# Performance work log

Hardware: AMD Instinct MI355X
Metric: run time of the kernel (lower is better)

Reference implementation:

```python
import jax, jax.numpy as jnp
import numpy as np

NEG_INF = -1.0e9  # matches module's negativeInfinity buffer


def setup_inputs() -> dict:
    key = jax.random.key(0)
    k0, k1, k2, k3 = jax.random.split(key, 4)
    bs, h, dh, qsl, sl = 2048, 8, 32, 64, 64
    q = jax.random.normal(k0, (bs, h, dh, qsl, 1), dtype=jnp.float32)
    k = jax.random.normal(k1, (bs, h, dh, 1, sl), dtype=jnp.float32)
    v = jax.random.normal(k2, (bs, h, dh, sl), dtype=jnp.float32)
    mask = jnp.zeros((bs, 1, qsl, sl), dtype=bool)
    gamma = jnp.ones((h,), dtype=jnp.float32)   # qk_GBN gamma
    bias = jax.random.normal(k3, (h,), dtype=jnp.float32) * 0.01  # qk_GBN bias
    return {"q": q, "k": k, "v": v, "mask": mask, "gamma": gamma, "bias": bias}


def reference(q, k, v, mask, gamma, bias):
    # scores: elementwise q*k summed over head-dim -> [bs, h, qsl, sl]
    qk = (q * k).sum(axis=2)
    # qk_GBN eval path: running m=0, s=1 -> per-head affine
    qk = qk * gamma[None, :, None, None] + bias[None, :, None, None]
    qk = jnp.where(mask, NEG_INF, qk)
    v_weights = jax.nn.softmax(qk, axis=-1)
    v_weights = jnp.where(mask, 0.0, v_weights)
    # sigmoid gating of attention weights
    v_weights = v_weights * jax.nn.sigmoid(qk)
    # output = v @ v_weights^T -> [bs, h, dvh, qsl]
    out = jnp.einsum("bhds,bhqs->bhdq", v, v_weights)
    return out
```

## Files before the change

kernel.cpp:

```cpp
#include <hip/hip_runtime.h>

typedef __attribute__((ext_vector_type(4))) float  f32x4;
typedef __attribute__((ext_vector_type(8))) __bf16 bf16x8;
typedef __attribute__((ext_vector_type(4))) __bf16 bf16x4;

#define MFMA16(a, b, c) __builtin_amdgcn_mfma_f32_16x16x32_bf16((a), (b), (c), 0, 0, 0)

__global__ __launch_bounds__(256, 8)
void mha_fused(const float* __restrict__ qg, const float* __restrict__ kg,
               const float* __restrict__ vg, const unsigned char* __restrict__ maskg,
               const float* __restrict__ gammag, const float* __restrict__ biasg,
               float* __restrict__ outg)
{
    const int bid = blockIdx.x;
    const int chunk = gridDim.x >> 3;
    const int bh = (bid & 7) * chunk + (bid >> 3);
    const int b  = bh >> 3;
    const int h  = bh & 7;
    const int t  = threadIdx.x;

    __shared__ __bf16 sKh[64][40];
    __shared__ __bf16 sKl[64][40];
    __shared__ __bf16 sV [32][72];

    const float* qb = qg + (size_t)bh * 2048;
    const float* kb = kg + (size_t)bh * 2048;
    const float* vb = vg + (size_t)bh * 2048;
    const unsigned char* mb = maskg + (size_t)b * 4096;
    float* ob = outg + (size_t)bh * 2048;

    const int w  = t >> 6;
    const int li = t & 15;
    const int hi = (t >> 4) & 3;
    const int i  = w * 16 + li;

    float qv[8];
    #pragma unroll
    for (int e = 0; e < 8; ++e) qv[e] = qb[(hi * 8 + e) * 64 + i];
    unsigned int mw[4];
    #pragma unroll
    for (int jt = 0; jt < 4; ++jt)
        mw[jt] = *(const unsigned int*)&mb[i * 64 + jt * 16 + hi * 4];

    {
        const int j = t & 63, sel = t >> 6;
        float a[8];
        #pragma unroll
        for (int e = 0; e < 8; ++e) a[e] = kb[(sel * 8 + e) * 64 + j];
        bf16x8 h8, l8;
        #pragma unroll
        for (int e = 0; e < 8; ++e) {
            __bf16 hh = (__bf16)a[e];
            h8[e] = hh;
            l8[e] = (__bf16)(a[e] - (float)hh);
        }
        const int slot = sel ^ ((j >> 3) & 3);
        *(bf16x8*)&sKh[j][slot * 8] = h8;
        *(bf16x8*)&sKl[j][slot * 8] = l8;
    }
    {
        const int d = t >> 3, j0 = (t & 7) * 8;
        f32x4 x0 = *(const f32x4*)&vb[d * 64 + j0];
        f32x4 x1 = *(const f32x4*)&vb[d * 64 + j0 + 4];
        bf16x8 vv = {(__bf16)x0[0], (__bf16)x0[1], (__bf16)x0[2], (__bf16)x0[3],
                     (__bf16)x1[0], (__bf16)x1[1], (__bf16)x1[2], (__bf16)x1[3]};
        *(bf16x8*)&sV[d][j0] = vv;
    }

    bf16x8 qh, ql;
    #pragma unroll
    for (int e = 0; e < 8; ++e) {
        __bf16 hh = (__bf16)qv[e];
        qh[e] = hh;
        ql[e] = (__bf16)(qv[e] - (float)hh);
    }

    __syncthreads();

    const float ga = gammag[h], be = biasg[h];
    float s[16];
    #pragma unroll
    for (int jt = 0; jt < 4; ++jt) {
        const int j = jt * 16 + li;
        const int slot = hi ^ ((j >> 3) & 3);
        bf16x8 ah = *(bf16x8*)&sKh[j][slot * 8];
        bf16x8 al = *(bf16x8*)&sKl[j][slot * 8];
        f32x4 c = {0.f, 0.f, 0.f, 0.f};
        c = MFMA16(al, qh, c);
        c = MFMA16(ah, ql, c);
        c = MFMA16(ah, qh, c);
        #pragma unroll
        for (int r = 0; r < 4; ++r) {
            float x = c[r] * ga + be;
            if ((mw[jt] >> (8 * r)) & 0xffu) x = -1.0e9f;
            s[jt * 4 + r] = x;
        }
    }

    float m = s[0];
    #pragma unroll
    for (int e = 1; e < 16; ++e) m = fmaxf(m, s[e]);
    m = fmaxf(m, __shfl_xor(m, 16));
    m = fmaxf(m, __shfl_xor(m, 32));
    float p[16], sum = 0.f;
    #pragma unroll
    for (int e = 0; e < 16; ++e) { p[e] = __expf(s[e] - m); sum += p[e]; }
    sum += __shfl_xor(sum, 16);
    sum += __shfl_xor(sum, 32);
    const float inv = 1.0f / sum;

    bf16x4 wv[4];
    #pragma unroll
    for (int jt = 0; jt < 4; ++jt) {
        #pragma unroll
        for (int r = 0; r < 4; ++r) {
            const int e = jt * 4 + r;
            const float g = 1.0f / (1.0f + __expf(-s[e]));
            wv[jt][r] = (__bf16)(p[e] * inv * g);
        }
    }

    f32x4 o0 = {0.f, 0.f, 0.f, 0.f};
    f32x4 o1 = {0.f, 0.f, 0.f, 0.f};
    #pragma unroll
    for (int kt = 0; kt < 2; ++kt) {
        bf16x4 wlo = wv[2 * kt], whi = wv[2 * kt + 1];
        bf16x8 wb = {wlo[0], wlo[1], wlo[2], wlo[3], whi[0], whi[1], whi[2], whi[3]};
        const int c0 = kt * 32 + hi * 4;
        const int c1 = kt * 32 + 16 + hi * 4;
        bf16x4 a0l = *(const bf16x4*)&sV[li][c0];
        bf16x4 a0h = *(const bf16x4*)&sV[li][c1];
        bf16x8 va = {a0l[0], a0l[1], a0l[2], a0l[3], a0h[0], a0h[1], a0h[2], a0h[3]};
        bf16x4 a1l = *(const bf16x4*)&sV[16 + li][c0];
        bf16x4 a1h = *(const bf16x4*)&sV[16 + li][c1];
        bf16x8 vc = {a1l[0], a1l[1], a1l[2], a1l[3], a1h[0], a1h[1], a1h[2], a1h[3]};
        o0 = MFMA16(va, wb, o0);
        o1 = MFMA16(vc, wb, o1);
    }
    #pragma unroll
    for (int r = 0; r < 4; ++r) {
        ob[(hi * 4 + r) * 64 + i]      = o0[r];
        ob[(16 + hi * 4 + r) * 64 + i] = o1[r];
    }
}

extern "C" void kernel_launch(void* const* d_in, const int* in_sizes, int n_in,
                              void* d_out, int out_size, void* d_ws, size_t ws_size,
                              hipStream_t stream)
{
    const float* q = (const float*)d_in[0];
    const float* k = (const float*)d_in[1];
    const float* v = (const float*)d_in[2];
    const unsigned char* mask = (const unsigned char*)d_in[3];
    const float* gamma = (const float*)d_in[4];
    const float* bias  = (const float*)d_in[5];
    float* out = (float*)d_out;

    const int num_bh = in_sizes[0] / 2048;
    dim3 grid(num_bh), block(256);
    hipLaunchKernelGGL(mha_fused, grid, block, 0, stream,
                       q, k, v, mask, gamma, bias, out);
}
```

Measured before the change: 110.0 us.

## Pack four heads per 1024-thread block and derive sigmoid from softmax exponentials

Each block now covers four heads of the same batch, with one 256-thread sub-block per head and per-head shared memory slices, so the grid is four times smaller. The sigmoid gate is rewritten as p/(p+exp(-m)), reusing the softmax exponential and removing one exp per element. Fewer, larger blocks cut scheduling overhead and share the mask rows across heads, but they may lower occupancy flexibility, and __syncthreads now spans 1024 threads. The algebraic sigmoid form can underflow when p and exp(-m) are both tiny.

```diff
diff --git a/kernel.cpp b/kernel.cpp
--- a/kernel.cpp
+++ b/kernel.cpp
@@ -6,22 +6,27 @@
 
 #define MFMA16(a, b, c) __builtin_amdgcn_mfma_f32_16x16x32_bf16((a), (b), (c), 0, 0, 0)
 
-__global__ __launch_bounds__(256, 8)
+__global__ __launch_bounds__(1024, 2)
 void mha_fused(const float* __restrict__ qg, const float* __restrict__ kg,
                const float* __restrict__ vg, const unsigned char* __restrict__ maskg,
                const float* __restrict__ gammag, const float* __restrict__ biasg,
                float* __restrict__ outg)
 {
-    const int bid = blockIdx.x;
+    const int bid   = blockIdx.x;
     const int chunk = gridDim.x >> 3;
-    const int bh = (bid & 7) * chunk + (bid >> 3);
-    const int b  = bh >> 3;
-    const int h  = bh & 7;
+    const int vbid  = (bid & 7) * chunk + (bid >> 3);
+    const int b  = vbid >> 1;
+    const int hg = vbid & 1;
+
     const int t  = threadIdx.x;
+    const int sb = t >> 8;
+    const int lt = t & 255;
+    const int h  = hg * 4 + sb;
+    const int bh = b * 8 + h;
 
-    __shared__ __bf16 sKh[64][40];
-    __shared__ __bf16 sKl[64][40];
-    __shared__ __bf16 sV [32][72];
+    __shared__ __bf16 sKh[4][64][40];
+    __shared__ __bf16 sKl[4][64][40];
+    __shared__ __bf16 sV [4][32][72];
 
     const float* qb = qg + (size_t)bh * 2048;
     const float* kb = kg + (size_t)bh * 2048;
@@ -29,9 +34,9 @@
     const unsigned char* mb = maskg + (size_t)b * 4096;
     float* ob = outg + (size_t)bh * 2048;
 
-    const int w  = t >> 6;
-    const int li = t & 15;
-    const int hi = (t >> 4) & 3;
+    const int w  = (lt >> 6) & 3;
+    const int li = lt & 15;
+    const int hi = (lt >> 4) & 3;
     const int i  = w * 16 + li;
 
     float qv[8];
@@ -43,7 +48,7 @@
         mw[jt] = *(const unsigned int*)&mb[i * 64 + jt * 16 + hi * 4];
 
     {
-        const int j = t & 63, sel = t >> 6;
+        const int j = lt & 63, sel = lt >> 6;
         float a[8];
         #pragma unroll
         for (int e = 0; e < 8; ++e) a[e] = kb[(sel * 8 + e) * 64 + j];
@@ -55,16 +60,16 @@
             l8[e] = (__bf16)(a[e] - (float)hh);
         }
         const int slot = sel ^ ((j >> 3) & 3);
-        *(bf16x8*)&sKh[j][slot * 8] = h8;
-        *(bf16x8*)&sKl[j][slot * 8] = l8;
+        *(bf16x8*)&sKh[sb][j][slot * 8] = h8;
+        *(bf16x8*)&sKl[sb][j][slot * 8] = l8;
     }
     {
-        const int d = t >> 3, j0 = (t & 7) * 8;
+        const int d = lt >> 3, j0 = (lt & 7) * 8;
         f32x4 x0 = *(const f32x4*)&vb[d * 64 + j0];
         f32x4 x1 = *(const f32x4*)&vb[d * 64 + j0 + 4];
         bf16x8 vv = {(__bf16)x0[0], (__bf16)x0[1], (__bf16)x0[2], (__bf16)x0[3],
                      (__bf16)x1[0], (__bf16)x1[1], (__bf16)x1[2], (__bf16)x1[3]};
-        *(bf16x8*)&sV[d][j0] = vv;
+        *(bf16x8*)&sV[sb][d][j0] = vv;
     }
 
     bf16x8 qh, ql;
@@ -83,8 +88,8 @@
     for (int jt = 0; jt < 4; ++jt) {
         const int j = jt * 16 + li;
         const int slot = hi ^ ((j >> 3) & 3);
-        bf16x8 ah = *(bf16x8*)&sKh[j][slot * 8];
-        bf16x8 al = *(bf16x8*)&sKl[j][slot * 8];
+        bf16x8 ah = *(bf16x8*)&sKh[sb][j][slot * 8];
+        bf16x8 al = *(bf16x8*)&sKl[sb][j][slot * 8];
         f32x4 c = {0.f, 0.f, 0.f, 0.f};
         c = MFMA16(al, qh, c);
         c = MFMA16(ah, ql, c);
@@ -102,9 +107,10 @@
     for (int e = 1; e < 16; ++e) m = fmaxf(m, s[e]);
     m = fmaxf(m, __shfl_xor(m, 16));
     m = fmaxf(m, __shfl_xor(m, 32));
-    float p[16], sum = 0.f;
+    const float em = __expf(-m);
+    float sum = 0.f;
     #pragma unroll
-    for (int e = 0; e < 16; ++e) { p[e] = __expf(s[e] - m); sum += p[e]; }
+    for (int e = 0; e < 16; ++e) { s[e] = __expf(s[e] - m); sum += s[e]; }
     sum += __shfl_xor(sum, 16);
     sum += __shfl_xor(sum, 32);
     const float inv = 1.0f / sum;
@@ -114,9 +120,8 @@
     for (int jt = 0; jt < 4; ++jt) {
         #pragma unroll
         for (int r = 0; r < 4; ++r) {
-            const int e = jt * 4 + r;
-            const float g = 1.0f / (1.0f + __expf(-s[e]));
-            wv[jt][r] = (__bf16)(p[e] * inv * g);
+            const float p = s[jt * 4 + r];
+            wv[jt][r] = (__bf16)(p * inv * __fdividef(p, p + em));
         }
     }
 
@@ -128,11 +133,11 @@
         bf16x8 wb = {wlo[0], wlo[1], wlo[2], wlo[3], whi[0], whi[1], whi[2], whi[3]};
         const int c0 = kt * 32 + hi * 4;
         const int c1 = kt * 32 + 16 + hi * 4;
-        bf16x4 a0l = *(const bf16x4*)&sV[li][c0];
-        bf16x4 a0h = *(const bf16x4*)&sV[li][c1];
+        bf16x4 a0l = *(const bf16x4*)&sV[sb][li][c0];
+        bf16x4 a0h = *(const bf16x4*)&sV[sb][li][c1];
         bf16x8 va = {a0l[0], a0l[1], a0l[2], a0l[3], a0h[0], a0h[1], a0h[2], a0h[3]};
-        bf16x4 a1l = *(const bf16x4*)&sV[16 + li][c0];
-        bf16x4 a1h = *(const bf16x4*)&sV[16 + li][c1];
+        bf16x4 a1l = *(const bf16x4*)&sV[sb][16 + li][c0];
+        bf16x4 a1h = *(const bf16x4*)&sV[sb][16 + li][c1];
         bf16x8 vc = {a1l[0], a1l[1], a1l[2], a1l[3], a1h[0], a1h[1], a1h[2], a1h[3]};
         o0 = MFMA16(va, wb, o0);
         o1 = MFMA16(vc, wb, o1);
@@ -157,7 +162,7 @@
     float* out = (float*)d_out;
 
     const int num_bh = in_sizes[0] / 2048;
-    dim3 grid(num_bh), block(256);
+    dim3 grid(num_bh >> 2), block(1024);
     hipLaunchKernelGGL(mha_fused, grid, block, 0, stream,
                        q, k, v, mask, gamma, bias, out);
 }
```

Measured after the change: 118.1 us. 1.07x slower.

## Stage Q/K/V/mask through LDS with vectorized loads and coalesced output stores

Applied to the files above, without the earlier changes.

Loads Q, K, V and the mask with contiguous 16-byte vector loads into shared memory, then transposes and splits them into bf16 hi/lo from LDS. Packs the mask into bit words and stages the output through LDS so the global stores are vectorized and coalesced. It also derives the sigmoid from the softmax exponentials (p/(p+e^-m)), which avoids a second exp, and drops the block-index swizzle and the occupancy hint. The cost is more LDS use, extra barriers and lower occupancy bounds.

```diff
diff --git a/kernel.cpp b/kernel.cpp
--- a/kernel.cpp
+++ b/kernel.cpp
@@ -1,80 +1,102 @@
 #include <hip/hip_runtime.h>
 
 typedef __attribute__((ext_vector_type(4))) float  f32x4;
+typedef __attribute__((ext_vector_type(2))) float  f32x2;
 typedef __attribute__((ext_vector_type(8))) __bf16 bf16x8;
 typedef __attribute__((ext_vector_type(4))) __bf16 bf16x4;
 
 #define MFMA16(a, b, c) __builtin_amdgcn_mfma_f32_16x16x32_bf16((a), (b), (c), 0, 0, 0)
 
-__global__ __launch_bounds__(256, 8)
+__global__ __launch_bounds__(256, 4)
 void mha_fused(const float* __restrict__ qg, const float* __restrict__ kg,
                const float* __restrict__ vg, const unsigned char* __restrict__ maskg,
                const float* __restrict__ gammag, const float* __restrict__ biasg,
                float* __restrict__ outg)
 {
-    const int bid = blockIdx.x;
-    const int chunk = gridDim.x >> 3;
-    const int bh = (bid & 7) * chunk + (bid >> 3);
+    const int bh = blockIdx.x;
     const int b  = bh >> 3;
     const int h  = bh & 7;
     const int t  = threadIdx.x;
 
-    __shared__ __bf16 sKh[64][40];
-    __shared__ __bf16 sKl[64][40];
-    __shared__ __bf16 sV [32][72];
+    __shared__ float              sQO[32 * 68];
+    __shared__ float              sKr[32 * 66];
+    __shared__ __bf16             sKh[64][40];
+    __shared__ __bf16             sKl[64][40];
+    __shared__ __bf16             sV [32][72];
+    __shared__ unsigned long long sMb[64];
 
     const float* qb = qg + (size_t)bh * 2048;
     const float* kb = kg + (size_t)bh * 2048;
     const float* vb = vg + (size_t)bh * 2048;
-    const unsigned char* mb = maskg + (size_t)b * 4096;
+    const unsigned char* mbp = maskg + (size_t)b * 4096;
     float* ob = outg + (size_t)bh * 2048;
 
     const int w  = t >> 6;
     const int li = t & 15;
     const int hi = (t >> 4) & 3;
     const int i  = w * 16 + li;
+    const int rd = t >> 3;
+    const int rc = (t & 7) * 8;
 
-    float qv[8];
+    {
+        f32x4 q0 = *(const f32x4*)(qb + t * 8);
+        f32x4 q1 = *(const f32x4*)(qb + t * 8 + 4);
+        f32x4 k0 = *(const f32x4*)(kb + t * 8);
+        f32x4 k1 = *(const f32x4*)(kb + t * 8 + 4);
+        f32x4 v0 = *(const f32x4*)(vb + t * 8);
+        f32x4 v1 = *(const f32x4*)(vb + t * 8 + 4);
+        uint4 mu = *(const uint4*)(mbp + t * 16);
+
+        float* qrow = &sQO[rd * 66 + rc];
+        *(f32x2*)(qrow + 0) = (f32x2){q0[0], q0[1]};
+        *(f32x2*)(qrow + 2) = (f32x2){q0[2], q0[3]};
+        *(f32x2*)(qrow + 4) = (f32x2){q1[0], q1[1]};
+        *(f32x2*)(qrow + 6) = (f32x2){q1[2], q1[3]};
+        float* krow = &sKr[rd * 66 + rc];
+        *(f32x2*)(krow + 0) = (f32x2){k0[0], k0[1]};
+        *(f32x2*)(krow + 2) = (f32x2){k0[2], k0[3]};
+        *(f32x2*)(krow + 4) = (f32x2){k1[0], k1[1]};
+        *(f32x2*)(krow + 6) = (f32x2){k1[2], k1[3]};
+
+        bf16x8 vv = {(__bf16)v0[0], (__bf16)v0[1], (__bf16)v0[2], (__bf16)v0[3],
+                     (__bf16)v1[0], (__bf16)v1[1], (__bf16)v1[2], (__bf16)v1[3]};
+        *(bf16x8*)&sV[rd][rc] = vv;
+
+        unsigned int n0 = ((mu.x & 0x01010101u) * 0x01020408u) >> 24;
+        unsigned int n1 = ((mu.y & 0x01010101u) * 0x01020408u) >> 24;
+        unsigned int n2 = ((mu.z & 0x01010101u) * 0x01020408u) >> 24;
+        unsigned int n3 = ((mu.w & 0x01010101u) * 0x01020408u) >> 24;
+        unsigned int n  = n0 | (n1 << 4) | (n2 << 8) | (n3 << 12);
+        ((unsigned short*)sMb)[(t >> 2) * 4 + (t & 3)] = (unsigned short)n;
+    }
+    __syncthreads();
+
+    bf16x8 qh, ql;
     #pragma unroll
-    for (int e = 0; e < 8; ++e) qv[e] = qb[(hi * 8 + e) * 64 + i];
-    unsigned int mw[4];
-    #pragma unroll
-    for (int jt = 0; jt < 4; ++jt)
-        mw[jt] = *(const unsigned int*)&mb[i * 64 + jt * 16 + hi * 4];
+    for (int e = 0; e < 8; ++e) {
+        const float a = sQO[(hi * 8 + e) * 66 + i];
+        const __bf16 hh = (__bf16)a;
+        qh[e] = hh;
+        ql[e] = (__bf16)(a - (float)hh);
+    }
+    const unsigned long long mrow = sMb[i];
+    const unsigned int mlo = (unsigned int)mrow;
+    const unsigned int mhw = (unsigned int)(mrow >> 32);
 
     {
         const int j = t & 63, sel = t >> 6;
-        float a[8];
-        #pragma unroll
-        for (int e = 0; e < 8; ++e) a[e] = kb[(sel * 8 + e) * 64 + j];
         bf16x8 h8, l8;
         #pragma unroll
         for (int e = 0; e < 8; ++e) {
-            __bf16 hh = (__bf16)a[e];
+            const float a = sKr[(sel * 8 + e) * 66 + j];
+            const __bf16 hh = (__bf16)a;
             h8[e] = hh;
-            l8[e] = (__bf16)(a[e] - (float)hh);
+            l8[e] = (__bf16)(a - (float)hh);
         }
         const int slot = sel ^ ((j >> 3) & 3);
         *(bf16x8*)&sKh[j][slot * 8] = h8;
         *(bf16x8*)&sKl[j][slot * 8] = l8;
     }
-    {
-        const int d = t >> 3, j0 = (t & 7) * 8;
-        f32x4 x0 = *(const f32x4*)&vb[d * 64 + j0];
-        f32x4 x1 = *(const f32x4*)&vb[d * 64 + j0 + 4];
-        bf16x8 vv = {(__bf16)x0[0], (__bf16)x0[1], (__bf16)x0[2], (__bf16)x0[3],
-                     (__bf16)x1[0], (__bf16)x1[1], (__bf16)x1[2], (__bf16)x1[3]};
-        *(bf16x8*)&sV[d][j0] = vv;
-    }
-
-    bf16x8 qh, ql;
-    #pragma unroll
-    for (int e = 0; e < 8; ++e) {
-        __bf16 hh = (__bf16)qv[e];
-        qh[e] = hh;
-        ql[e] = (__bf16)(qv[e] - (float)hh);
-    }
-
     __syncthreads();
 
     const float ga = gammag[h], be = biasg[h];
@@ -89,10 +111,12 @@
         c = MFMA16(al, qh, c);
         c = MFMA16(ah, ql, c);
         c = MFMA16(ah, qh, c);
+        const unsigned int mword = (jt & 2) ? mhw : mlo;
+        const unsigned int mnib  = mword >> ((jt & 1) * 16 + hi * 4);
         #pragma unroll
         for (int r = 0; r < 4; ++r) {
             float x = c[r] * ga + be;
-            if ((mw[jt] >> (8 * r)) & 0xffu) x = -1.0e9f;
+            if ((mnib >> r) & 1u) x = -1.0e9f;
             s[jt * 4 + r] = x;
         }
     }
@@ -102,9 +126,10 @@
     for (int e = 1; e < 16; ++e) m = fmaxf(m, s[e]);
     m = fmaxf(m, __shfl_xor(m, 16));
     m = fmaxf(m, __shfl_xor(m, 32));
-    float p[16], sum = 0.f;
+    const float em = __expf(-m);
+    float sum = 0.f;
     #pragma unroll
-    for (int e = 0; e < 16; ++e) { p[e] = __expf(s[e] - m); sum += p[e]; }
+    for (int e = 0; e < 16; ++e) { s[e] = __expf(s[e] - m); sum += s[e]; }
     sum += __shfl_xor(sum, 16);
     sum += __shfl_xor(sum, 32);
     const float inv = 1.0f / sum;
@@ -114,9 +139,8 @@
     for (int jt = 0; jt < 4; ++jt) {
         #pragma unroll
         for (int r = 0; r < 4; ++r) {
-            const int e = jt * 4 + r;
-            const float g = 1.0f / (1.0f + __expf(-s[e]));
-            wv[jt][r] = (__bf16)(p[e] * inv * g);
+            const float p = s[jt * 4 + r];
+            wv[jt][r] = (__bf16)(p * inv * __fdividef(p, p + em));
         }
     }
 
@@ -124,8 +148,8 @@
     f32x4 o1 = {0.f, 0.f, 0.f, 0.f};
     #pragma unroll
     for (int kt = 0; kt < 2; ++kt) {
-        bf16x4 wlo = wv[2 * kt], whi = wv[2 * kt + 1];
-        bf16x8 wb = {wlo[0], wlo[1], wlo[2], wlo[3], whi[0], whi[1], whi[2], whi[3]};
+        bf16x4 wlo = wv[2 * kt], whi2 = wv[2 * kt + 1];
+        bf16x8 wb = {wlo[0], wlo[1], wlo[2], wlo[3], whi2[0], whi2[1], whi2[2], whi2[3]};
         const int c0 = kt * 32 + hi * 4;
         const int c1 = kt * 32 + 16 + hi * 4;
         bf16x4 a0l = *(const bf16x4*)&sV[li][c0];
@@ -137,10 +161,18 @@
         o0 = MFMA16(va, wb, o0);
         o1 = MFMA16(vc, wb, o1);
     }
+
     #pragma unroll
     for (int r = 0; r < 4; ++r) {
-        ob[(hi * 4 + r) * 64 + i]      = o0[r];
-        ob[(16 + hi * 4 + r) * 64 + i] = o1[r];
+        sQO[(hi * 4 + r) * 68 + i]      = o0[r];
+        sQO[(16 + hi * 4 + r) * 68 + i] = o1[r];
+    }
+    __syncthreads();
+    {
+        f32x4 r0 = *(const f32x4*)&sQO[rd * 68 + rc];
+        f32x4 r1 = *(const f32x4*)&sQO[rd * 68 + rc + 4];
+        *(f32x4*)(ob + t * 8)     = r0;
+        *(f32x4*)(ob + t * 8 + 4) = r1;
     }
 }
 
```

After: 105.1 us. 4.5% less time.

## Process all heads per block with register-prefetched next head

Applied to the files above, without the earlier changes.

Each block now handles one batch element and loops over its 8 heads, so the mask loads once per batch instead of once per head. While computing the current head, the block prefetches the next head's Q/K/V into registers and converts them into shared memory between two barriers. The sigmoid is rewritten to reuse the softmax exponent via p/(p+exp(-m)), which saves one exp per element. The grid is 8x smaller (2048 blocks) and launch bounds drop to 5 waves, which trades occupancy and parallelism for software pipelining and adds two barriers per head.

```diff
diff --git a/kernel.cpp b/kernel.cpp
--- a/kernel.cpp
+++ b/kernel.cpp
@@ -6,141 +6,171 @@
 
 #define MFMA16(a, b, c) __builtin_amdgcn_mfma_f32_16x16x32_bf16((a), (b), (c), 0, 0, 0)
 
-__global__ __launch_bounds__(256, 8)
+__global__ __launch_bounds__(256, 5)
 void mha_fused(const float* __restrict__ qg, const float* __restrict__ kg,
                const float* __restrict__ vg, const unsigned char* __restrict__ maskg,
                const float* __restrict__ gammag, const float* __restrict__ biasg,
                float* __restrict__ outg)
 {
-    const int bid = blockIdx.x;
-    const int chunk = gridDim.x >> 3;
-    const int bh = (bid & 7) * chunk + (bid >> 3);
-    const int b  = bh >> 3;
-    const int h  = bh & 7;
-    const int t  = threadIdx.x;
+    const int b = blockIdx.x;
+    const int t = threadIdx.x;
 
     __shared__ __bf16 sKh[64][40];
     __shared__ __bf16 sKl[64][40];
     __shared__ __bf16 sV [32][72];
 
-    const float* qb = qg + (size_t)bh * 2048;
-    const float* kb = kg + (size_t)bh * 2048;
-    const float* vb = vg + (size_t)bh * 2048;
-    const unsigned char* mb = maskg + (size_t)b * 4096;
-    float* ob = outg + (size_t)bh * 2048;
+    const size_t base = (size_t)b * 8 * 2048;
+    const unsigned char* mbp = maskg + (size_t)b * 4096;
 
-    const int w  = t >> 6;
     const int li = t & 15;
     const int hi = (t >> 4) & 3;
+    const int w  = t >> 6;
     const int i  = w * 16 + li;
+    const int jK = t & 63;
+    const int slotW = (w ^ ((jK >> 3) & 3)) * 8;
+    const int vd = t >> 3, vj = (t & 7) * 8;
 
-    float qv[8];
-    #pragma unroll
-    for (int e = 0; e < 8; ++e) qv[e] = qb[(hi * 8 + e) * 64 + i];
     unsigned int mw[4];
     #pragma unroll
     for (int jt = 0; jt < 4; ++jt)
-        mw[jt] = *(const unsigned int*)&mb[i * 64 + jt * 16 + hi * 4];
+        mw[jt] = *(const unsigned int*)&mbp[i * 64 + jt * 16 + hi * 4];
 
+    float kv[8], qv[8];
+    f32x4 v0x, v1x;
     {
-        const int j = t & 63, sel = t >> 6;
-        float a[8];
+        const float* kb = kg + base;
         #pragma unroll
-        for (int e = 0; e < 8; ++e) a[e] = kb[(sel * 8 + e) * 64 + j];
+        for (int e = 0; e < 8; ++e) kv[e] = kb[(w * 8 + e) * 64 + jK];
+        const float* vb = vg + base;
+        v0x = *(const f32x4*)(vb + t * 8);
+        v1x = *(const f32x4*)(vb + t * 8 + 4);
+        const float* qb = qg + base;
+        #pragma unroll
+        for (int e = 0; e < 8; ++e) qv[e] = qb[(hi * 8 + e) * 64 + i];
+    }
+    bf16x8 qh, ql;
+    {
         bf16x8 h8, l8;
         #pragma unroll
         for (int e = 0; e < 8; ++e) {
-            __bf16 hh = (__bf16)a[e];
-            h8[e] = hh;
-            l8[e] = (__bf16)(a[e] - (float)hh);
+            const __bf16 hh = (__bf16)kv[e];
+            h8[e] = hh; l8[e] = (__bf16)(kv[e] - (float)hh);
         }
-        const int slot = sel ^ ((j >> 3) & 3);
-        *(bf16x8*)&sKh[j][slot * 8] = h8;
-        *(bf16x8*)&sKl[j][slot * 8] = l8;
+        *(bf16x8*)&sKh[jK][slotW] = h8;
+        *(bf16x8*)&sKl[jK][slotW] = l8;
+        bf16x8 vv = {(__bf16)v0x[0], (__bf16)v0x[1], (__bf16)v0x[2], (__bf16)v0x[3],
+                     (__bf16)v1x[0], (__bf16)v1x[1], (__bf16)v1x[2], (__bf16)v1x[3]};
+        *(bf16x8*)&sV[vd][vj] = vv;
+        #pragma unroll
+        for (int e = 0; e < 8; ++e) {
+            const __bf16 hh = (__bf16)qv[e];
+            qh[e] = hh; ql[e] = (__bf16)(qv[e] - (float)hh);
+        }
     }
-    {
-        const int d = t >> 3, j0 = (t & 7) * 8;
-        f32x4 x0 = *(const f32x4*)&vb[d * 64 + j0];
-        f32x4 x1 = *(const f32x4*)&vb[d * 64 + j0 + 4];
-        bf16x8 vv = {(__bf16)x0[0], (__bf16)x0[1], (__bf16)x0[2], (__bf16)x0[3],
-                     (__bf16)x1[0], (__bf16)x1[1], (__bf16)x1[2], (__bf16)x1[3]};
-        *(bf16x8*)&sV[d][j0] = vv;
-    }
-
-    bf16x8 qh, ql;
-    #pragma unroll
-    for (int e = 0; e < 8; ++e) {
-        __bf16 hh = (__bf16)qv[e];
-        qh[e] = hh;
-        ql[e] = (__bf16)(qv[e] - (float)hh);
-    }
-
     __syncthreads();
 
-    const float ga = gammag[h], be = biasg[h];
-    float s[16];
-    #pragma unroll
-    for (int jt = 0; jt < 4; ++jt) {
-        const int j = jt * 16 + li;
-        const int slot = hi ^ ((j >> 3) & 3);
-        bf16x8 ah = *(bf16x8*)&sKh[j][slot * 8];
-        bf16x8 al = *(bf16x8*)&sKl[j][slot * 8];
-        f32x4 c = {0.f, 0.f, 0.f, 0.f};
-        c = MFMA16(al, qh, c);
-        c = MFMA16(ah, ql, c);
-        c = MFMA16(ah, qh, c);
+    #pragma unroll 1
+    for (int p = 0; p < 8; ++p) {
+        float kvn[8], qvn[8];
+        f32x4 v0n, v1n;
+        const bool pre = (p < 7);
+        if (pre) {
+            const size_t nb = base + (size_t)(p + 1) * 2048;
+            const float* kb = kg + nb;
+            #pragma unroll
+            for (int e = 0; e < 8; ++e) kvn[e] = kb[(w * 8 + e) * 64 + jK];
+            const float* vb = vg + nb;
+            v0n = *(const f32x4*)(vb + t * 8);
+            v1n = *(const f32x4*)(vb + t * 8 + 4);
+            const float* qb = qg + nb;
+            #pragma unroll
+            for (int e = 0; e < 8; ++e) qvn[e] = qb[(hi * 8 + e) * 64 + i];
+        }
+
+        const float ga = gammag[p], be = biasg[p];
+        float s[16];
+        #pragma unroll
+        for (int jt = 0; jt < 4; ++jt) {
+            const int j = jt * 16 + li;
+            const int slot = (hi ^ ((j >> 3) & 3)) * 8;
+            bf16x8 ah = *(bf16x8*)&sKh[j][slot];
+            bf16x8 al = *(bf16x8*)&sKl[j][slot];
+            f32x4 c = {0.f, 0.f, 0.f, 0.f};
+            c = MFMA16(al, qh, c);
+            c = MFMA16(ah, ql, c);
+            c = MFMA16(ah, qh, c);
+            #pragma unroll
+            for (int r = 0; r < 4; ++r) {
+                float x = c[r] * ga + be;
+                if ((mw[jt] >> (8 * r)) & 0xffu) x = -1.0e9f;
+                s[jt * 4 + r] = x;
+            }
+        }
+        float m = s[0];
+        #pragma unroll
+        for (int e = 1; e < 16; ++e) m = fmaxf(m, s[e]);
+        m = fmaxf(m, __shfl_xor(m, 16));
+        m = fmaxf(m, __shfl_xor(m, 32));
+        const float em = __expf(-m);
+        float sum = 0.f;
+        #pragma unroll
+        for (int e = 0; e < 16; ++e) { s[e] = __expf(s[e] - m); sum += s[e]; }
+        sum += __shfl_xor(sum, 16);
+        sum += __shfl_xor(sum, 32);
+        const float inv = 1.0f / sum;
+
+        bf16x4 wv[4];
+        #pragma unroll
+        for (int jt = 0; jt < 4; ++jt) {
+            #pragma unroll
+            for (int r = 0; r < 4; ++r) {
+                const float pp = s[jt * 4 + r];
+                wv[jt][r] = (__bf16)(pp * inv * __fdividef(pp, pp + em));
+            }
+        }
+
+        f32x4 o0 = {0.f, 0.f, 0.f, 0.f}, o1 = {0.f, 0.f, 0.f, 0.f};
+        #pragma unroll
+        for (int kt = 0; kt < 2; ++kt) {
+            bf16x4 wlo = wv[2 * kt], whi2 = wv[2 * kt + 1];
+            bf16x8 wb = {wlo[0], wlo[1], wlo[2], wlo[3], whi2[0], whi2[1], whi2[2], whi2[3]};
+            const int c0 = kt * 32 + hi * 4, c1 = kt * 32 + 16 + hi * 4;
+            bf16x4 a0l = *(const bf16x4*)&sV[li][c0];
+            bf16x4 a0h = *(const bf16x4*)&sV[li][c1];
+            bf16x8 va = {a0l[0], a0l[1], a0l[2], a0l[3], a0h[0], a0h[1], a0h[2], a0h[3]};
+            bf16x4 a1l = *(const bf16x4*)&sV[16 + li][c0];
+            bf16x4 a1h = *(const bf16x4*)&sV[16 + li][c1];
+            bf16x8 vc = {a1l[0], a1l[1], a1l[2], a1l[3], a1h[0], a1h[1], a1h[2], a1h[3]};
+            o0 = MFMA16(va, wb, o0);
+            o1 = MFMA16(vc, wb, o1);
+        }
+        float* ob = outg + base + (size_t)p * 2048;
         #pragma unroll
         for (int r = 0; r < 4; ++r) {
-            float x = c[r] * ga + be;
-            if ((mw[jt] >> (8 * r)) & 0xffu) x = -1.0e9f;
-            s[jt * 4 + r] = x;
+            ob[(hi * 4 + r) * 64 + i]      = o0[r];
+            ob[(16 + hi * 4 + r) * 64 + i] = o1[r];
         }
-    }
 
-    float m = s[0];
-    #pragma unroll
-    for (int e = 1; e < 16; ++e) m = fmaxf(m, s[e]);
-    m = fmaxf(m, __shfl_xor(m, 16));
-    m = fmaxf(m, __shfl_xor(m, 32));
-    float p[16], sum = 0.f;
-    #pragma unroll
-    for (int e = 0; e < 16; ++e) { p[e] = __expf(s[e] - m); sum += p[e]; }
-    sum += __shfl_xor(sum, 16);
-    sum += __shfl_xor(sum, 32);
-    const float inv = 1.0f / sum;
-
-    bf16x4 wv[4];
-    #pragma unroll
-    for (int jt = 0; jt < 4; ++jt) {
-        #pragma unroll
-        for (int r = 0; r < 4; ++r) {
-            const int e = jt * 4 + r;
-            const float g = 1.0f / (1.0f + __expf(-s[e]));
-            wv[jt][r] = (__bf16)(p[e] * inv * g);
+        if (pre) {
+            __syncthreads();
+            bf16x8 h8, l8;
+            #pragma unroll
+            for (int e = 0; e < 8; ++e) {
+                const __bf16 hh = (__bf16)kvn[e];
+                h8[e] = hh; l8[e] = (__bf16)(kvn[e] - (float)hh);
+            }
+            *(bf16x8*)&sKh[jK][slotW] = h8;
+            *(bf16x8*)&sKl[jK][slotW] = l8;
+            bf16x8 vv = {(__bf16)v0n[0], (__bf16)v0n[1], (__bf16)v0n[2], (__bf16)v0n[3],
+                         (__bf16)v1n[0], (__bf16)v1n[1], (__bf16)v1n[2], (__bf16)v1n[3]};
+            *(bf16x8*)&sV[vd][vj] = vv;
+            #pragma unroll
+            for (int e = 0; e < 8; ++e) {
+                const __bf16 hh = (__bf16)qvn[e];
+                qh[e] = hh; ql[e] = (__bf16)(qvn[e] - (float)hh);
+            }
+            __syncthreads();
         }
-    }
-
-    f32x4 o0 = {0.f, 0.f, 0.f, 0.f};
-    f32x4 o1 = {0.f, 0.f, 0.f, 0.f};
-    #pragma unroll
-    for (int kt = 0; kt < 2; ++kt) {
-        bf16x4 wlo = wv[2 * kt], whi = wv[2 * kt + 1];
-        bf16x8 wb = {wlo[0], wlo[1], wlo[2], wlo[3], whi[0], whi[1], whi[2], whi[3]};
-        const int c0 = kt * 32 + hi * 4;
-        const int c1 = kt * 32 + 16 + hi * 4;
-        bf16x4 a0l = *(const bf16x4*)&sV[li][c0];
-        bf16x4 a0h = *(const bf16x4*)&sV[li][c1];
-        bf16x8 va = {a0l[0], a0l[1], a0l[2], a0l[3], a0h[0], a0h[1], a0h[2], a0h[3]};
-        bf16x4 a1l = *(const bf16x4*)&sV[16 + li][c0];
-        bf16x4 a1h = *(const bf16x4*)&sV[16 + li][c1];
-        bf16x8 vc = {a1l[0], a1l[1], a1l[2], a1l[3], a1h[0], a1h[1], a1h[2], a1h[3]};
-        o0 = MFMA16(va, wb, o0);
-        o1 = MFMA16(vc, wb, o1);
-    }
-    #pragma unroll
-    for (int r = 0; r < 4; ++r) {
-        ob[(hi * 4 + r) * 64 + i]      = o0[r];
-        ob[(16 + hi * 4 + r) * 64 + i] = o1[r];
     }
 }
 
@@ -157,7 +187,7 @@
     float* out = (float*)d_out;
 
     const int num_bh = in_sizes[0] / 2048;
-    dim3 grid(num_bh), block(256);
+    dim3 grid(num_bh >> 3), block(256);
     hipLaunchKernelGGL(mha_fused, grid, block, 0, stream,
                        q, k, v, mask, gamma, bias, out);
 }
```

Result: slower. 117.9 us (+7.2%).
